# Kernel tuning notes

Measured on AMD Instinct MI355X. Metric: run time of the kernel, lower is better.

Reference implementation:

```python
import jax, jax.numpy as jnp
import numpy as np

TEMPERATURE = 8.0  # sqrt(head_dim=64)
B, LQ, LK, D = 8, 512, 512, 64


def setup_inputs() -> dict:
    key = jax.random.key(0)
    kq, kk, kv, kb = jax.random.split(key, 4)
    return {
        "q": jax.random.normal(kq, (B, LQ, D), dtype=jnp.float32),
        "k": jax.random.normal(kk, (B, LK, D), dtype=jnp.float32),
        "v": jax.random.normal(kv, (B, LK, D), dtype=jnp.float32),
        "bias": jax.random.normal(kb, (B, LQ, LK, D), dtype=jnp.float32),
    }


def reference(q, k, v, bias):
    # attn1[b,i,j] = q . k ; attn2[b,i,j] = q[b,i] . bias[b,i,j]
    scores = (jnp.einsum('bid,bjd->bij', q, k)
              + jnp.einsum('bid,bijd->bij', q, bias)) / TEMPERATURE
    attn = jax.nn.softmax(scores, axis=2)  # [B, LQ, LK]
    # dropout is identity in eval/deterministic reference
    # emb1 = attn @ v ; emb2[b,i] = sum_j attn[b,i,j] * bias[b,i,j,:]
    output = (jnp.einsum('bij,bjd->bid', attn, v)
              + jnp.einsum('bij,bijd->bid', attn, bias))
    return (output, attn)
```

## Files before the change

### kernel.cpp

```cpp
#include <hip/hip_runtime.h>

#define BB 8
#define LQ 512
#define LK 512
#define DD 64

constexpr float SCALE_LOG2E = 0.125f * 1.44269504088896340736f;

typedef float f32x2 __attribute__((ext_vector_type(2)));

__global__ __launch_bounds__(256) void attn_bias_kernel(
    const float* __restrict__ q,
    const float* __restrict__ k,
    const float* __restrict__ v,
    const float* __restrict__ bias,
    float* __restrict__ out_emb,
    float* __restrict__ out_attn)
{
    const int row  = blockIdx.x;
    const int b    = row >> 9;
    const int tid  = threadIdx.x;
    const int wave = tid >> 6;
    const int lane = tid & 63;
    const int jj   = lane >> 4;
    const int t    = lane & 15;
    const int g    = (wave << 2) | jj;

    __shared__ float  w_lds[LK];
    __shared__ float4 o_lds4[16 * 16];
    __shared__ float  l_lds[16];

    const float4 qf = reinterpret_cast<const float4*>(q + row * DD)[t];

    const float4* bias_row = reinterpret_cast<const float4*>(
        bias + (size_t)row * (LK * DD));
    const float4* k_b = reinterpret_cast<const float4*>(k + b * (LK * DD));
    const float4* v_b = reinterpret_cast<const float4*>(v + b * (LK * DD));

    float  l = 0.f;
    float4 o = make_float4(0.f, 0.f, 0.f, 0.f);

    #pragma unroll 4
    for (int it = 0; it < LK / 16; ++it) {
        const int j   = (it << 4) + g;
        const int idx = j * (DD / 4) + t;
        const float4 bv = bias_row[idx];
        const float4 kv = k_b[idx];
        const float4 vv = v_b[idx];

        float part = qf.x * (kv.x + bv.x)
                   + qf.y * (kv.y + bv.y)
                   + qf.z * (kv.z + bv.z)
                   + qf.w * (kv.w + bv.w);
        part += __shfl_xor(part, 1);
        part += __shfl_xor(part, 2);
        part += __shfl_xor(part, 4);
        part += __shfl_xor(part, 8);

        const float w = __builtin_amdgcn_exp2f(part * SCALE_LOG2E);
        if (t == 0) w_lds[j] = w;

        l += w;
        o.x += w * (vv.x + bv.x);
        o.y += w * (vv.y + bv.y);
        o.z += w * (vv.z + bv.z);
        o.w += w * (vv.w + bv.w);
    }

    o_lds4[g * 16 + t] = o;
    if (t == 0) l_lds[g] = l;
    __syncthreads();

    float L = 0.f;
    #pragma unroll
    for (int gg = 0; gg < 16; ++gg) L += l_lds[gg];
    const float invL = 1.0f / L;

    {
        const f32x2* w2 = reinterpret_cast<const f32x2*>(w_lds);
        f32x2* attn_row2 = reinterpret_cast<f32x2*>(
            out_attn + (size_t)row * LK);
        f32x2 val = w2[tid];
        val.x *= invL;
        val.y *= invL;
        __builtin_nontemporal_store(val, &attn_row2[tid]);
    }

    if (tid < DD) {
        const float* o_f = reinterpret_cast<const float*>(o_lds4);
        float O = 0.f;
        #pragma unroll
        for (int gg = 0; gg < 16; ++gg)
            O += o_f[gg * DD + tid];
        out_emb[row * DD + tid] = O * invL;
    }
}

extern "C" void kernel_launch(void* const* d_in, const int* in_sizes, int n_in,
                              void* d_out, int out_size, void* d_ws, size_t ws_size,
                              hipStream_t stream) {
    const float* q    = (const float*)d_in[0];
    const float* k    = (const float*)d_in[1];
    const float* v    = (const float*)d_in[2];
    const float* bias = (const float*)d_in[3];
    float* out_emb  = (float*)d_out;
    float* out_attn = (float*)d_out + BB * LQ * DD;

    attn_bias_kernel<<<BB * LQ, 256, 0, stream>>>(q, k, v, bias, out_emb, out_attn);
}
```

Before: 702.0 us.

## Split attention into separate K, bias, and V passes with staggered order

Splits the fused loop into three passes: q·k scores into shared memory, then a bias pass that computes weights and accumulates bias-weighted output, then a V accumulation pass reading the stored weights. K and V passes rotate their iteration order by row to spread cache accesses across blocks. Bias is read with nontemporal loads, so the streaming bias traffic is less likely to evict the reused K/V data. This adds extra barriers and shared-memory traffic.

```diff
diff --git a/kernel.cpp b/kernel.cpp
--- a/kernel.cpp
+++ b/kernel.cpp
@@ -8,6 +8,7 @@
 constexpr float SCALE_LOG2E = 0.125f * 1.44269504088896340736f;
 
 typedef float f32x2 __attribute__((ext_vector_type(2)));
+typedef float f32x4 __attribute__((ext_vector_type(4)));
 
 __global__ __launch_bounds__(256) void attn_bias_kernel(
     const float* __restrict__ q,
@@ -26,48 +27,69 @@
     const int t    = lane & 15;
     const int g    = (wave << 2) | jj;
 
-    __shared__ float  w_lds[LK];
-    __shared__ float4 o_lds4[16 * 16];
-    __shared__ float  l_lds[16];
+    __shared__ float s1_lds[LK];
+    __shared__ float w_lds[LK];
+    __shared__ f32x4 o_lds[16 * 16];
+    __shared__ float l_lds[16];
 
-    const float4 qf = reinterpret_cast<const float4*>(q + row * DD)[t];
+    const f32x4 qf = reinterpret_cast<const f32x4*>(q + row * DD)[t];
 
-    const float4* bias_row = reinterpret_cast<const float4*>(
+    const f32x4* bias_row = reinterpret_cast<const f32x4*>(
         bias + (size_t)row * (LK * DD));
-    const float4* k_b = reinterpret_cast<const float4*>(k + b * (LK * DD));
-    const float4* v_b = reinterpret_cast<const float4*>(v + b * (LK * DD));
-
-    float  l = 0.f;
-    float4 o = make_float4(0.f, 0.f, 0.f, 0.f);
+    const f32x4* k_b = reinterpret_cast<const f32x4*>(k + b * (LK * DD));
+    const f32x4* v_b = reinterpret_cast<const f32x4*>(v + b * (LK * DD));
 
     #pragma unroll 4
-    for (int it = 0; it < LK / 16; ++it) {
-        const int j   = (it << 4) + g;
-        const int idx = j * (DD / 4) + t;
-        const float4 bv = bias_row[idx];
-        const float4 kv = k_b[idx];
-        const float4 vv = v_b[idx];
-
-        float part = qf.x * (kv.x + bv.x)
-                   + qf.y * (kv.y + bv.y)
-                   + qf.z * (kv.z + bv.z)
-                   + qf.w * (kv.w + bv.w);
+    for (int it0 = 0; it0 < LK / 16; ++it0) {
+        const int it = (it0 + row) & 31;
+        const int j  = (it << 4) + g;
+        const f32x4 kv = k_b[j * (DD / 4) + t];
+        float part = qf.x * kv.x + qf.y * kv.y + qf.z * kv.z + qf.w * kv.w;
         part += __shfl_xor(part, 1);
         part += __shfl_xor(part, 2);
         part += __shfl_xor(part, 4);
         part += __shfl_xor(part, 8);
+        if (t == 0) s1_lds[j] = part;
+    }
+    __syncthreads();
 
-        const float w = __builtin_amdgcn_exp2f(part * SCALE_LOG2E);
+    float l = 0.f;
+    f32x4 o = {0.f, 0.f, 0.f, 0.f};
+
+    #pragma unroll 4
+    for (int it = 0; it < LK / 16; ++it) {
+        const int j = (it << 4) + g;
+        const f32x4 bv =
+            __builtin_nontemporal_load(&bias_row[j * (DD / 4) + t]);
+        float part = qf.x * bv.x + qf.y * bv.y + qf.z * bv.z + qf.w * bv.w;
+        part += __shfl_xor(part, 1);
+        part += __shfl_xor(part, 2);
+        part += __shfl_xor(part, 4);
+        part += __shfl_xor(part, 8);
+        const float s1j = s1_lds[j];
+        const float w = __builtin_amdgcn_exp2f((part + s1j) * SCALE_LOG2E);
         if (t == 0) w_lds[j] = w;
+        l += w;
+        o.x += w * bv.x;
+        o.y += w * bv.y;
+        o.z += w * bv.z;
+        o.w += w * bv.w;
+    }
+    __syncthreads();
 
-        l += w;
-        o.x += w * (vv.x + bv.x);
-        o.y += w * (vv.y + bv.y);
-        o.z += w * (vv.z + bv.z);
-        o.w += w * (vv.w + bv.w);
+    #pragma unroll 4
+    for (int it0 = 0; it0 < LK / 16; ++it0) {
+        const int it = (it0 + row) & 31;
+        const int j  = (it << 4) + g;
+        const f32x4 vv = v_b[j * (DD / 4) + t];
+        const float w  = w_lds[j];
+        o.x += w * vv.x;
+        o.y += w * vv.y;
+        o.z += w * vv.z;
+        o.w += w * vv.w;
     }
 
-    o_lds4[g * 16 + t] = o;
+    o_lds[g * 16 + t] = o;
     if (t == 0) l_lds[g] = l;
     __syncthreads();
 
@@ -87,7 +109,7 @@
     }
 
     if (tid < DD) {
-        const float* o_f = reinterpret_cast<const float*>(o_lds4);
+        const float* o_f = reinterpret_cast<const float*>(o_lds);
         float O = 0.f;
         #pragma unroll
         for (int gg = 0; gg < 16; ++gg)
```

Result: no change. 697.5 us (-0.7%).
